# Performance work log

Hardware: AMD Instinct MI355X
Metric: run time of the kernel (lower is better)

## Reference

```python
import jax, jax.numpy as jnp
import numpy as np

B, T, H, V = 64, 512, 300, 50257


def setup_inputs() -> dict:
    key = jax.random.key(0)
    k0, k1, k2, k3, k4 = jax.random.split(key, 5)
    tokens = jax.random.randint(k0, (B, T), 0, V, dtype=jnp.int32)
    ihs = jnp.zeros((B, H), jnp.float32)
    emb = jax.random.normal(k1, (V, H), jnp.float32) * 0.02
    W = jax.random.normal(k2, (H, H), jnp.float32) * (1.0 / np.sqrt(H))
    U = jax.random.normal(k3, (H, H), jnp.float32) * (1.0 / np.sqrt(H))
    Wout = jax.random.normal(k4, (V, H), jnp.float32) * 0.02
    bout = jnp.zeros((V,), jnp.float32)
    return {"ihs": ihs, "tokens": tokens, "emb": emb, "W": W, "U": U,
            "Wout": Wout, "bout": bout}


def reference(ihs, tokens, emb, W, U, Wout, bout):
    # Embedding lookup: [B, T, H]
    x = emb[tokens]
    # Precompute input projection for all timesteps: U x_t (Linear: x @ U^T)
    ux = jnp.einsum('bth,gh->btg', x, U)  # [B, T, H]
    ux_tmajor = jnp.swapaxes(ux, 0, 1)    # [T, B, H]

    def step(h, ux_t):
        # h_t = tanh(W h_{t-1} + U x_t)
        h_next = jnp.tanh(h @ W.T + ux_t)
        return h_next, h_next

    h_last, _ = jax.lax.scan(step, ihs, ux_tmajor)
    # final hidden state -> vocab logits
    logits = h_last @ Wout.T + bout  # [B, V]
    return logits
```

## Files before the change

kernel.cpp:

```cpp
#include <hip/hip_runtime.h>
#include <math.h>

#define H 300
#define BB 64
#define TT 512
#define VV 50257
#define KC 30

__global__ void transpose_k(const float* __restrict__ in, float* __restrict__ out) {
    int idx = blockIdx.x * blockDim.x + threadIdx.x;
    if (idx < H * H) {
        int r = idx / H, c = idx - r * H;
        out[idx] = in[c * H + r];
    }
}

__global__ __launch_bounds__(256) void ux_k(const int* __restrict__ tokens,
                                            const float* __restrict__ emb,
                                            const float* __restrict__ Ut,
                                            float* __restrict__ ux) {
    __shared__ __align__(16) float x_s[KC][BB];
    __shared__ __align__(16) float ut_s[KC][304];
    __shared__ int tok_s[BB];

    const int t = blockIdx.x;
    const int tid = threadIdx.x;
    if (tid < BB) tok_s[tid] = tokens[tid * TT + t];

    const int tb = tid >> 4;
    const int tg = tid & 15;
    const int b0 = tb * 4;
    const int g0 = tg * 20;
    const bool active = (tg < 15);

    float acc[4][20];
#pragma unroll
    for (int i = 0; i < 4; ++i)
#pragma unroll
        for (int j = 0; j < 20; ++j) acc[i][j] = 0.f;

    __syncthreads();

    for (int h0 = 0; h0 < H; h0 += KC) {
        for (int i = tid; i < BB * 32; i += 256) {
            int b = i >> 5, k = i & 31;
            if (k < KC) x_s[k][b] = emb[tok_s[b] * H + h0 + k];
        }
        for (int i = tid; i < KC * H; i += 256) {
            int k = i / H, g = i - k * H;
            ut_s[k][g] = Ut[(h0 + k) * H + g];
        }
        __syncthreads();
        if (active) {
#pragma unroll 2
            for (int k = 0; k < KC; ++k) {
                float4 xa = *reinterpret_cast<const float4*>(&x_s[k][b0]);
                float4 u0 = *reinterpret_cast<const float4*>(&ut_s[k][g0 + 0]);
                float4 u1 = *reinterpret_cast<const float4*>(&ut_s[k][g0 + 4]);
                float4 u2 = *reinterpret_cast<const float4*>(&ut_s[k][g0 + 8]);
                float4 u3 = *reinterpret_cast<const float4*>(&ut_s[k][g0 + 12]);
                float4 u4 = *reinterpret_cast<const float4*>(&ut_s[k][g0 + 16]);
                const float xr[4] = {xa.x, xa.y, xa.z, xa.w};
                const float ur[20] = {u0.x, u0.y, u0.z, u0.w,
                                      u1.x, u1.y, u1.z, u1.w,
                                      u2.x, u2.y, u2.z, u2.w,
                                      u3.x, u3.y, u3.z, u3.w,
                                      u4.x, u4.y, u4.z, u4.w};
#pragma unroll
                for (int i = 0; i < 4; ++i)
#pragma unroll
                    for (int j = 0; j < 20; ++j)
                        acc[i][j] += xr[i] * ur[j];
            }
        }
        __syncthreads();
    }

    if (active) {
#pragma unroll
        for (int i = 0; i < 4; ++i) {
            float* dst = ux + (t * BB + b0 + i) * H + g0;
#pragma unroll
            for (int jq = 0; jq < 5; ++jq) {
                *reinterpret_cast<float4*>(dst + jq * 4) =
                    make_float4(acc[i][jq * 4 + 0], acc[i][jq * 4 + 1],
                                acc[i][jq * 4 + 2], acc[i][jq * 4 + 3]);
            }
        }
    }
}

#define RNN_REP19(X) X(0) X(1) X(2) X(3) X(4) X(5) X(6) X(7) X(8) X(9) \
    X(10) X(11) X(12) X(13) X(14) X(15) X(16) X(17) X(18)

__global__ __attribute__((amdgpu_flat_work_group_size(512, 512), amdgpu_waves_per_eu(2, 2)))
void rnn_k(const float* __restrict__ W,
           const float* __restrict__ ux,
           const float* __restrict__ ihs,
           float* __restrict__ hlast) {
    __shared__ __align__(16) float4 wl4_s[450 * 11];
    __shared__ __align__(16) float h_s[304];
    __shared__ float p_s[608];
    const int b = blockIdx.x;
    const int tid = threadIdx.x;
    const int tt = (tid < 450) ? tid : 449;
    const int c = tt / 150;
    const int g2 = tt - c * 150;

    const float4* wrA4 = reinterpret_cast<const float4*>(W + (size_t)g2 * H + c * 100);
    const float4* wrB4 = reinterpret_cast<const float4*>(W + (size_t)(g2 + 150) * H + c * 100);

#define RNN_WA(q) float4 wa##q = wrA4[q];
    RNN_REP19(RNN_WA)
#undef RNN_WA
#define RNN_WB(q) float4 wb##q = wrB4[q];
    RNN_REP19(RNN_WB)
#undef RNN_WB
    float4 wb19 = wrB4[19];

    const int wbase = tt * 11;
#pragma unroll
    for (int i = 0; i < 6; ++i) wl4_s[wbase + i] = wrA4[19 + i];
#pragma unroll
    for (int i = 0; i < 5; ++i) wl4_s[wbase + 6 + i] = wrB4[20 + i];

    if (tid < H) h_s[tid] = ihs[b * H + tid];

    const float* uxb = ux + b * H;
    float u0 = 0.f, u1 = 0.f;
    if (tid < 150) {
        u0 = uxb[g2];
        u1 = uxb[150 + g2];
    }
    __syncthreads();

    const float4* hs4 = reinterpret_cast<const float4*>(h_s);
    const int hoff = c * 25;

#pragma unroll 1
    for (int t = 0; t < TT; ++t) {
        float n0 = 0.f, n1 = 0.f;
        if (tid < 150 && t + 1 < TT) {
            const float* nx = uxb + (t + 1) * (BB * H);
            n0 = nx[g2];
            n1 = nx[150 + g2];
        }
        float accA0 = 0.f, accA1 = 0.f, accA2 = 0.f, accA3 = 0.f;
        float accB0 = 0.f, accB1 = 0.f, accB2 = 0.f, accB3 = 0.f;
#define RNN_Q(q) { float4 h4 = hs4[hoff + q]; \
        accA0 += wa##q.x * h4.x; accA1 += wa##q.y * h4.y; \
        accA2 += wa##q.z * h4.z; accA3 += wa##q.w * h4.w; \
        accB0 += wb##q.x * h4.x; accB1 += wb##q.y * h4.y; \
        accB2 += wb##q.z * h4.z; accB3 += wb##q.w * h4.w; }
        RNN_REP19(RNN_Q)
#undef RNN_Q
        {
            float4 h4 = hs4[hoff + 19];
            float4 wA = wl4_s[wbase + 0];
            accA0 += wA.x * h4.x; accA1 += wA.y * h4.y;
            accA2 += wA.z * h4.z; accA3 += wA.w * h4.w;
            accB0 += wb19.x * h4.x; accB1 += wb19.y * h4.y;
            accB2 += wb19.z * h4.z; accB3 += wb19.w * h4.w;
        }
#pragma unroll
        for (int q = 20; q < 25; ++q) {
            float4 h4 = hs4[hoff + q];
            float4 wA = wl4_s[wbase + (q - 19)];
            float4 wB = wl4_s[wbase + 6 + (q - 20)];
            accA0 += wA.x * h4.x; accA1 += wA.y * h4.y;
            accA2 += wA.z * h4.z; accA3 += wA.w * h4.w;
            accB0 += wB.x * h4.x; accB1 += wB.y * h4.y;
            accB2 += wB.z * h4.z; accB3 += wB.w * h4.w;
        }
        float accA = (accA0 + accA1) + (accA2 + accA3);
        float accB = (accB0 + accB1) + (accB2 + accB3);
        if (tid < 450 && c == 1) { p_s[g2] = accA; p_s[150 + g2] = accB; }
        if (tid < 450 && c == 2) { p_s[304 + g2] = accA; p_s[454 + g2] = accB; }
        __syncthreads();
        if (tid < 150) {
            float z0 = accA + p_s[g2] + p_s[304 + g2] + u0;
            float z1 = accB + p_s[150 + g2] + p_s[454 + g2] + u1;
            float e0 = __expf(2.f * z0);
            float e1 = __expf(2.f * z1);
            h_s[g2]       = 1.f - 2.f * __builtin_amdgcn_rcpf(e0 + 1.f);
            h_s[150 + g2] = 1.f - 2.f * __builtin_amdgcn_rcpf(e1 + 1.f);
        }
        u0 = n0; u1 = n1;
        __syncthreads();
    }
    if (tid < H) hlast[b * H + tid] = h_s[tid];
}

__global__ __launch_bounds__(256) void logits_k(const float* __restrict__ hlast,
                                                const float* __restrict__ Wout,
                                                const float* __restrict__ bout,
                                                float* __restrict__ out) {
    __shared__ __align__(16) float Ws[32 * 132];
    __shared__ __align__(16) float hs[32 * 76];
    const int tid = threadIdx.x;
    const int tv = tid & 31;
    const int tb = tid >> 5;
    const int v0 = blockIdx.x * 128;

    float acc[8][4];
#pragma unroll
    for (int i = 0; i < 8; ++i)
#pragma unroll
        for (int j = 0; j < 4; ++j) acc[i][j] = 0.f;

    for (int hb = 0; hb < H; hb += 32) {
        __syncthreads();
        {
            const int vp = tid >> 1;
            const int hloc = (tid & 1) * 16;
            int vv = v0 + vp; if (vv > VV - 1) vv = VV - 1;
            const float* wrow = Wout + (size_t)vv * H + hb + hloc;
#pragma unroll
            for (int i = 0; i < 4; ++i) {
                const int hg = hb + hloc + i * 4;
                float4 val;
                if (hg + 3 < H) {
                    val = *reinterpret_cast<const float4*>(wrow + i * 4);
                } else {
                    val.x = (hg + 0 < H) ? wrow[i * 4 + 0] : 0.f;
                    val.y = (hg + 1 < H) ? wrow[i * 4 + 1] : 0.f;
                    val.z = (hg + 2 < H) ? wrow[i * 4 + 2] : 0.f;
                    val.w = (hg + 3 < H) ? wrow[i * 4 + 3] : 0.f;
                }
                Ws[(hloc + i * 4 + 0) * 132 + vp] = val.x;
                Ws[(hloc + i * 4 + 1) * 132 + vp] = val.y;
                Ws[(hloc + i * 4 + 2) * 132 + vp] = val.z;
                Ws[(hloc + i * 4 + 3) * 132 + vp] = val.w;
            }
        }
        {
            const int bb = tid >> 2;
            const int hl = (tid & 3) * 8;
            const float* hrow = hlast + bb * H + hb + hl;
#pragma unroll
            for (int i = 0; i < 2; ++i) {
                const int hg = hb + hl + i * 4;
                float4 val;
                if (hg + 3 < H) {
                    val = *reinterpret_cast<const float4*>(hrow + i * 4);
                } else {
                    val.x = (hg + 0 < H) ? hrow[i * 4 + 0] : 0.f;
                    val.y = (hg + 1 < H) ? hrow[i * 4 + 1] : 0.f;
                    val.z = (hg + 2 < H) ? hrow[i * 4 + 2] : 0.f;
                    val.w = (hg + 3 < H) ? hrow[i * 4 + 3] : 0.f;
                }
                hs[(hl + i * 4 + 0) * 76 + bb] = val.x;
                hs[(hl + i * 4 + 1) * 76 + bb] = val.y;
                hs[(hl + i * 4 + 2) * 76 + bb] = val.z;
                hs[(hl + i * 4 + 3) * 76 + bb] = val.w;
            }
        }
        __syncthreads();
        const float4* Ws4 = reinterpret_cast<const float4*>(Ws);
        const float4* hs4 = reinterpret_cast<const float4*>(hs);
#pragma unroll
        for (int h2 = 0; h2 < 32; ++h2) {
            float4 w4  = Ws4[h2 * 33 + tv];
            float4 h4a = hs4[h2 * 19 + tb * 2];
            float4 h4b = hs4[h2 * 19 + tb * 2 + 1];
            const float hv[8] = {h4a.x, h4a.y, h4a.z, h4a.w,
                                 h4b.x, h4b.y, h4b.z, h4b.w};
#pragma unroll
            for (int bi = 0; bi < 8; ++bi) {
                acc[bi][0] += hv[bi] * w4.x;
                acc[bi][1] += hv[bi] * w4.y;
                acc[bi][2] += hv[bi] * w4.z;
                acc[bi][3] += hv[bi] * w4.w;
            }
        }
    }

    const int vg = v0 + tv * 4;
    float4 bq;
    if (vg + 3 < VV) bq = *reinterpret_cast<const float4*>(bout + vg);
    else {
        bq.x = (vg + 0 < VV) ? bout[vg + 0] : 0.f;
        bq.y = (vg + 1 < VV) ? bout[vg + 1] : 0.f;
        bq.z = (vg + 2 < VV) ? bout[vg + 2] : 0.f;
        bq.w = (vg + 3 < VV) ? bout[vg + 3] : 0.f;
    }
#pragma unroll
    for (int bi = 0; bi < 8; ++bi) {
        const int bb = tb * 8 + bi;
        float* op = out + (size_t)bb * VV + vg;
        if (vg + 0 < VV) op[0] = acc[bi][0] + bq.x;
        if (vg + 1 < VV) op[1] = acc[bi][1] + bq.y;
        if (vg + 2 < VV) op[2] = acc[bi][2] + bq.z;
        if (vg + 3 < VV) op[3] = acc[bi][3] + bq.w;
    }
}

extern "C" void kernel_launch(void* const* d_in, const int* in_sizes, int n_in,
                              void* d_out, int out_size, void* d_ws, size_t ws_size,
                              hipStream_t stream) {
    const float* ihs    = (const float*)d_in[0];
    const int*   tokens = (const int*)  d_in[1];
    const float* emb    = (const float*)d_in[2];
    const float* W      = (const float*)d_in[3];
    const float* U      = (const float*)d_in[4];
    const float* Wout   = (const float*)d_in[5];
    const float* bout   = (const float*)d_in[6];
    float* out = (float*)d_out;

    char* ws = (char*)d_ws;
    float* Ut    = (float*)(ws + 0);
    float* hlast = (float*)(ws + 400000);
    float* ux    = (float*)(ws + 1048576);

    const int tp_blocks = (H * H + 255) / 256;
    transpose_k<<<tp_blocks, 256, 0, stream>>>(U, Ut);
    ux_k<<<TT, 256, 0, stream>>>(tokens, emb, Ut, ux);
    rnn_k<<<BB, 512, 0, stream>>>(W, ux, ihs, hlast);
    logits_k<<<(VV + 127) / 128, 256, 0, stream>>>(hlast, Wout, bout, out);
}
```

Baseline: 811.5 us.

## Keep full W slice in registers in RNN kernel; rebalance ux GEMM column mapping

The recurrent kernel now holds all 25 float4 pairs of each thread's W rows in VGPRs, pinned with empty asm constraints, instead of spilling the tail into a shared-memory array. This removes the per-step LDS reads of weights, at the cost of much higher register pressure (200 VGPRs for weights), which could cause spills. It also enlarges p_s to about 80KB, apparently to limit occupancy to one block per CU. The ux projection kernel is changed so all 16 column-group threads participate with an interleaved float4 column mapping instead of idling one in sixteen.

```diff
diff --git a/kernel.cpp b/kernel.cpp
--- a/kernel.cpp
+++ b/kernel.cpp
@@ -30,8 +30,6 @@
     const int tb = tid >> 4;
     const int tg = tid & 15;
     const int b0 = tb * 4;
-    const int g0 = tg * 20;
-    const bool active = (tg < 15);
 
     float acc[4][20];
 #pragma unroll
@@ -51,56 +49,56 @@
             ut_s[k][g] = Ut[(h0 + k) * H + g];
         }
         __syncthreads();
-        if (active) {
 #pragma unroll 2
-            for (int k = 0; k < KC; ++k) {
-                float4 xa = *reinterpret_cast<const float4*>(&x_s[k][b0]);
-                float4 u0 = *reinterpret_cast<const float4*>(&ut_s[k][g0 + 0]);
-                float4 u1 = *reinterpret_cast<const float4*>(&ut_s[k][g0 + 4]);
-                float4 u2 = *reinterpret_cast<const float4*>(&ut_s[k][g0 + 8]);
-                float4 u3 = *reinterpret_cast<const float4*>(&ut_s[k][g0 + 12]);
-                float4 u4 = *reinterpret_cast<const float4*>(&ut_s[k][g0 + 16]);
-                const float xr[4] = {xa.x, xa.y, xa.z, xa.w};
-                const float ur[20] = {u0.x, u0.y, u0.z, u0.w,
-                                      u1.x, u1.y, u1.z, u1.w,
-                                      u2.x, u2.y, u2.z, u2.w,
-                                      u3.x, u3.y, u3.z, u3.w,
-                                      u4.x, u4.y, u4.z, u4.w};
-#pragma unroll
-                for (int i = 0; i < 4; ++i)
-#pragma unroll
-                    for (int j = 0; j < 20; ++j)
-                        acc[i][j] += xr[i] * ur[j];
-            }
-        }
-        __syncthreads();
-    }
-
-    if (active) {
-#pragma unroll
-        for (int i = 0; i < 4; ++i) {
-            float* dst = ux + (t * BB + b0 + i) * H + g0;
-#pragma unroll
-            for (int jq = 0; jq < 5; ++jq) {
-                *reinterpret_cast<float4*>(dst + jq * 4) =
-                    make_float4(acc[i][jq * 4 + 0], acc[i][jq * 4 + 1],
-                                acc[i][jq * 4 + 2], acc[i][jq * 4 + 3]);
-            }
-        }
-    }
-}
-
-#define RNN_REP19(X) X(0) X(1) X(2) X(3) X(4) X(5) X(6) X(7) X(8) X(9) \
-    X(10) X(11) X(12) X(13) X(14) X(15) X(16) X(17) X(18)
+        for (int k = 0; k < KC; ++k) {
+            float4 xa = *reinterpret_cast<const float4*>(&x_s[k][b0]);
+            const float* ur = &ut_s[k][0];
+            float4 u[5];
+#pragma unroll
+            for (int j = 0; j < 5; ++j) {
+                const int q = tg + 16 * j;
+                u[j] = (q < 75) ? *reinterpret_cast<const float4*>(ur + 4 * q)
+                                : make_float4(0.f, 0.f, 0.f, 0.f);
+            }
+            const float xr[4] = {xa.x, xa.y, xa.z, xa.w};
+#pragma unroll
+            for (int i = 0; i < 4; ++i)
+#pragma unroll
+                for (int j = 0; j < 5; ++j) {
+                    acc[i][4 * j + 0] += xr[i] * u[j].x;
+                    acc[i][4 * j + 1] += xr[i] * u[j].y;
+                    acc[i][4 * j + 2] += xr[i] * u[j].z;
+                    acc[i][4 * j + 3] += xr[i] * u[j].w;
+                }
+        }
+        __syncthreads();
+    }
+
+#pragma unroll
+    for (int i = 0; i < 4; ++i) {
+        float* dst = ux + (t * BB + b0 + i) * H;
+#pragma unroll
+        for (int j = 0; j < 5; ++j) {
+            const int q = tg + 16 * j;
+            if (q < 75)
+                *reinterpret_cast<float4*>(dst + 4 * q) =
+                    make_float4(acc[i][4 * j + 0], acc[i][4 * j + 1],
+                                acc[i][4 * j + 2], acc[i][4 * j + 3]);
+        }
+    }
+}
+
+#define RNN_REP25(X) X(0) X(1) X(2) X(3) X(4) X(5) X(6) X(7) X(8) X(9) \
+    X(10) X(11) X(12) X(13) X(14) X(15) X(16) X(17) X(18) X(19) \
+    X(20) X(21) X(22) X(23) X(24)
 
 __global__ __attribute__((amdgpu_flat_work_group_size(512, 512), amdgpu_waves_per_eu(2, 2)))
 void rnn_k(const float* __restrict__ W,
            const float* __restrict__ ux,
            const float* __restrict__ ihs,
            float* __restrict__ hlast) {
-    __shared__ __align__(16) float4 wl4_s[450 * 11];
     __shared__ __align__(16) float h_s[304];
-    __shared__ float p_s[608];
+    __shared__ float p_s[20608];
     const int b = blockIdx.x;
     const int tid = threadIdx.x;
     const int tt = (tid < 450) ? tid : 449;
@@ -110,19 +108,13 @@
     const float4* wrA4 = reinterpret_cast<const float4*>(W + (size_t)g2 * H + c * 100);
     const float4* wrB4 = reinterpret_cast<const float4*>(W + (size_t)(g2 + 150) * H + c * 100);
 
-#define RNN_WA(q) float4 wa##q = wrA4[q];
-    RNN_REP19(RNN_WA)
-#undef RNN_WA
-#define RNN_WB(q) float4 wb##q = wrB4[q];
-    RNN_REP19(RNN_WB)
-#undef RNN_WB
-    float4 wb19 = wrB4[19];
-
-    const int wbase = tt * 11;
-#pragma unroll
-    for (int i = 0; i < 6; ++i) wl4_s[wbase + i] = wrA4[19 + i];
-#pragma unroll
-    for (int i = 0; i < 5; ++i) wl4_s[wbase + 6 + i] = wrB4[20 + i];
+#define RNN_DECL(q) float4 wa##q = wrA4[q]; float4 wb##q = wrB4[q];
+    RNN_REP25(RNN_DECL)
+#undef RNN_DECL
+#define RNN_PIN(q) asm("" : "+v"(wa##q.x), "+v"(wa##q.y), "+v"(wa##q.z), "+v"(wa##q.w), \
+                           "+v"(wb##q.x), "+v"(wb##q.y), "+v"(wb##q.z), "+v"(wb##q.w));
+    RNN_REP25(RNN_PIN)
+#undef RNN_PIN
 
     if (tid < H) h_s[tid] = ihs[b * H + tid];
 
@@ -152,26 +144,8 @@
         accA2 += wa##q.z * h4.z; accA3 += wa##q.w * h4.w; \
         accB0 += wb##q.x * h4.x; accB1 += wb##q.y * h4.y; \
         accB2 += wb##q.z * h4.z; accB3 += wb##q.w * h4.w; }
-        RNN_REP19(RNN_Q)
+        RNN_REP25(RNN_Q)
 #undef RNN_Q
-        {
-            float4 h4 = hs4[hoff + 19];
-            float4 wA = wl4_s[wbase + 0];
-            accA0 += wA.x * h4.x; accA1 += wA.y * h4.y;
-            accA2 += wA.z * h4.z; accA3 += wA.w * h4.w;
-            accB0 += wb19.x * h4.x; accB1 += wb19.y * h4.y;
-            accB2 += wb19.z * h4.z; accB3 += wb19.w * h4.w;
-        }
-#pragma unroll
-        for (int q = 20; q < 25; ++q) {
-            float4 h4 = hs4[hoff + q];
-            float4 wA = wl4_s[wbase + (q - 19)];
-            float4 wB = wl4_s[wbase + 6 + (q - 20)];
-            accA0 += wA.x * h4.x; accA1 += wA.y * h4.y;
-            accA2 += wA.z * h4.z; accA3 += wA.w * h4.w;
-            accB0 += wB.x * h4.x; accB1 += wB.y * h4.y;
-            accB2 += wB.z * h4.z; accB3 += wB.w * h4.w;
-        }
         float accA = (accA0 + accA1) + (accA2 + accA3);
         float accB = (accB0 + accB1) + (accB2 + accB3);
         if (tid < 450 && c == 1) { p_s[g2] = accA; p_s[150 + g2] = accB; }
```

Measured after the change: 911.2 us. 12.3% more time.
